# Kernel optimization log

Hardware: AMD Instinct MI355X
Metric: run time of the kernel (lower is better)

Reference implementation:

```python
import jax, jax.numpy as jnp
import numpy as np

V = [8192, 2048, 512, 128, 32]   # vertex counts per mesh level
S = 9                            # spiral length
T = 64                           # number of audio frames
OC = [32, 64, 64, 128]           # out_channels
LAT = 64                         # latent_channels


def _spiral_conv(x, idx, w, b):
    # x: [B, Vi, C], idx: [Vi, S] -> gather spiral neighborhoods, flatten, linear
    B = x.shape[0]
    n, s = idx.shape
    g = x[:, idx.reshape(-1), :].reshape(B, n, -1)  # [B, Vi, S*C]
    return g @ w + b


def _pool(x, row, col, val, out_size):
    # sparse COO matmul along vertex dim: out[b, r, :] += val * x[b, c, :]
    g = x[:, col, :] * val[None, :, None]
    return jnp.zeros((x.shape[0], out_size, x.shape[2]), x.dtype).at[:, row, :].add(g)


def setup_inputs():
    key = jax.random.key(0)
    keys = iter(jax.random.split(key, 80))
    def nrm(shape, scale=0.05):
        return jax.random.normal(next(keys), shape, jnp.float32) * scale
    inp = {}
    inp["hidden_states"] = jax.random.normal(next(keys), (1, T, 768), jnp.float32)
    inp["actor"] = jax.random.normal(next(keys), (1, V[0], 3), jnp.float32)
    inp["audio_w"] = nrm((768, LAT)); inp["audio_b"] = jnp.zeros((LAT,), jnp.float32)
    enc_dims = [(3 * S, OC[0]), (OC[0] * S, OC[1]), (OC[1] * S, OC[2]), (OC[2] * S, OC[3])]
    for i, (a, b) in enumerate(enc_dims):
        inp[f"enc{i}_w"] = nrm((a, b)); inp[f"enc{i}_b"] = jnp.zeros((b,), jnp.float32)
    inp["enc_lat_w"] = nrm((V[4] * OC[3], LAT)); inp["enc_lat_b"] = jnp.zeros((LAT,), jnp.float32)
    inp["dec_lin_w"] = nrm((2 * LAT, V[4] * OC[3])); inp["dec_lin_b"] = jnp.zeros((V[4] * OC[3],), jnp.float32)
    dec_dims = [(OC[3] * S, OC[3]), (OC[3] * S, OC[2]), (OC[2] * S, OC[1]), (OC[1] * S, OC[0])]
    for i, (a, b) in enumerate(dec_dims):
        inp[f"dec{i}_w"] = nrm((a, b)); inp[f"dec{i}_b"] = jnp.zeros((b,), jnp.float32)
    inp["dec_out_w"] = nrm((OC[0] * S, 3)); inp["dec_out_b"] = jnp.zeros((3,), jnp.float32)
    for i in range(4):
        inp[f"spiral{i}"] = jax.random.randint(next(keys), (V[i], S), 0, V[i])
    for i in range(4):
        vin, vout = V[i], V[i + 1]
        inp[f"down{i}_row"] = jnp.repeat(jnp.arange(vout), 3)
        inp[f"down{i}_col"] = jax.random.randint(next(keys), (3 * vout,), 0, vin)
        inp[f"down{i}_val"] = jax.random.uniform(next(keys), (3 * vout,), jnp.float32) / 3.0
        inp[f"up{i}_row"] = jnp.repeat(jnp.arange(vin), 3)
        inp[f"up{i}_col"] = jax.random.randint(next(keys), (3 * vin,), 0, vout)
        inp[f"up{i}_val"] = jax.random.uniform(next(keys), (3 * vin,), jnp.float32) / 3.0
    return inp


def reference(hidden_states, actor, audio_w, audio_b,
              enc0_w, enc0_b, enc1_w, enc1_b, enc2_w, enc2_b, enc3_w, enc3_b,
              enc_lat_w, enc_lat_b,
              dec_lin_w, dec_lin_b, dec0_w, dec0_b, dec1_w, dec1_b,
              dec2_w, dec2_b, dec3_w, dec3_b, dec_out_w, dec_out_b,
              spiral0, spiral1, spiral2, spiral3,
              down0_row, down0_col, down0_val, down1_row, down1_col, down1_val,
              down2_row, down2_col, down2_val, down3_row, down3_col, down3_val,
              up0_row, up0_col, up0_val, up1_row, up1_col, up1_val,
              up2_row, up2_col, up2_val, up3_row, up3_col, up3_val):
    spirals = [spiral0, spiral1, spiral2, spiral3]
    enc_p = [(enc0_w, enc0_b), (enc1_w, enc1_b), (enc2_w, enc2_b), (enc3_w, enc3_b)]
    dec_p = [(dec0_w, dec0_b), (dec1_w, dec1_b), (dec2_w, dec2_b), (dec3_w, dec3_b)]
    down = [(down0_row, down0_col, down0_val), (down1_row, down1_col, down1_val),
            (down2_row, down2_col, down2_val), (down3_row, down3_col, down3_val)]
    up = [(up0_row, up0_col, up0_val), (up1_row, up1_col, up1_val),
          (up2_row, up2_col, up2_val), (up3_row, up3_col, up3_val)]

    # ---- encode(actor): conv -> elu -> pool per level, then flatten linear ----
    x = actor  # [1, V0, 3]
    for i in range(4):
        w, b = enc_p[i]
        x = jax.nn.elu(_spiral_conv(x, spirals[i], w, b))
        r, c, v = down[i]
        x = _pool(x, r, c, v, V[i + 1])
    actor_emb = x.reshape(1, -1) @ enc_lat_w + enc_lat_b  # [1, LAT]

    # ---- audio embedding and latent concat ----
    audio_emb = hidden_states[0] @ audio_w + audio_b       # [T, LAT]
    latent = jnp.concatenate(
        [audio_emb, jnp.broadcast_to(actor_emb, audio_emb.shape)], axis=-1)  # [T, 2*LAT]

    # ---- decode all frames at once (original loops per frame; batched over T) ----
    x = (latent @ dec_lin_w + dec_lin_b).reshape(-1, V[4], OC[3])  # [T, V4, OC3]
    for i in range(4):
        lvl = 3 - i
        r, c, v = up[lvl]
        x = _pool(x, r, c, v, V[lvl])
        w, b = dec_p[i]
        x = jax.nn.elu(_spiral_conv(x, spirals[lvl], w, b))
    x = _spiral_conv(x, spirals[0], dec_out_w, dec_out_b)  # [T, V0, 3]
    return x + actor  # broadcast actor (displacement prediction), pred_sequence[1:]
```

## Files before the change

### kernel.cpp

```cpp
#include <hip/hip_runtime.h>
#include <hip/hip_bf16.h>

typedef __hip_bfloat16 bf16;
typedef __attribute__((ext_vector_type(8))) short short8v;
typedef __attribute__((ext_vector_type(16))) float f32x16;

__device__ __forceinline__ float tof(float v){ return v; }
__device__ __forceinline__ float tof(bf16 v){ return __bfloat162float(v); }
__device__ __forceinline__ void sto(float* p, float v){ *p = v; }
__device__ __forceinline__ void sto(bf16* p, float v){ *p = __float2bfloat16(v); }
__device__ __forceinline__ short f2bs(float f){ bf16 h = __float2bfloat16(f); return *(short*)&h; }
__device__ __forceinline__ float bsu2f(short s){
    return __uint_as_float(((unsigned)(unsigned short)s) << 16);
}

__device__ __forceinline__ void sto4(float* p, float4 v){ *(float4*)p = v; }
__device__ __forceinline__ void sto4(bf16* p, float4 v){
    short4 s; s.x=f2bs(v.x); s.y=f2bs(v.y); s.z=f2bs(v.z); s.w=f2bs(v.w);
    *(short4*)p = s;
}

__device__ __forceinline__ void swz_t(int b, int bs, int& t, int& rem){
    int x = b & 7, k = b >> 3;
    t = x*8 + (k >> bs);
    rem = k & ((1 << bs) - 1);
}

__global__ __launch_bounds__(256) void k_prep(
    const float* __restrict__ w0, const float* __restrict__ w1,
    const float* __restrict__ w2, const float* __restrict__ w3,
    const float* __restrict__ w4,
    short* __restrict__ wt0, short* __restrict__ wt1,
    short* __restrict__ wt2, short* __restrict__ wt3,
    short* __restrict__ wt4,
    const float* __restrict__ hs, const float* __restrict__ aw,
    const float* __restrict__ ab, float* __restrict__ aemb)
{
    __shared__ float red[4][64];
    int b = blockIdx.x, tid = threadIdx.x;
    if (b < 1080){
        const float* w; short* wt; int K, nsh, i;
        if      (b < 576) { w = w0; wt = wt0; K = 1152; nsh = 7; i = b*256 + tid; }
        else if (b < 864) { w = w1; wt = wt1; K = 1152; nsh = 6; i = (b-576)*256 + tid; }
        else if (b < 1008){ w = w2; wt = wt2; K = 576;  nsh = 6; i = (b-864)*256 + tid; }
        else              { w = w3; wt = wt3; K = 576;  nsh = 5; i = (b-1008)*256 + tid; }
        int k = i >> nsh, n = i & ((1 << nsh) - 1);
        wt[n*K + k] = f2bs(w[i]);
    } else if (b < 1116){
        int i = (b - 1080)*256 + tid;
        int k = i >> 5, n = i & 31;
        wt4[n*288 + k] = (n < 3) ? f2bs(w4[k*3 + n]) : (short)0;
    } else {
        int t = b - 1116;
        int kg = tid >> 6, l = tid & 63;
        const float* h = hs + t*768;
        float acc = 0.f;
        int k0 = kg*192;
        #pragma unroll 8
        for (int k = k0; k < k0 + 192; k++) acc += h[k] * aw[k*64 + l];
        red[kg][l] = acc;
        __syncthreads();
        if (kg == 0)
            aemb[t*64 + l] = red[0][l] + red[1][l] + red[2][l] + red[3][l] + ab[l];
    }
}

__global__ __launch_bounds__(256) void k_enclat(const float* __restrict__ flat,
    const float* __restrict__ w, const float* __restrict__ b, float* __restrict__ out)
{
    __shared__ float red[256];
    int l = blockIdx.x, tid = threadIdx.x;
    float acc = 0.f;
    for (int k = tid; k < 4096; k += 256) acc += flat[k] * w[k*64 + l];
    red[tid] = acc; __syncthreads();
    for (int s = 128; s > 0; s >>= 1){ if (tid < s) red[tid] += red[tid+s]; __syncthreads(); }
    if (tid == 0) out[l] = red[0] + b[l];
}

__global__ __launch_bounds__(256) void k_declin4(const float* __restrict__ ae,
    const float* __restrict__ pe, const float* __restrict__ w, const float* __restrict__ b,
    bf16* __restrict__ out)
{
    int n4 = blockIdx.x*256 + threadIdx.x;
    int t = blockIdx.y;
    float4 acc = *(const float4*)&b[n4*4];
    const float* a = ae + t*64;
    #pragma unroll 4
    for (int k = 0; k < 64; k++){
        float av = a[k];
        float4 wv = *(const float4*)&w[(size_t)k*4096 + n4*4];
        acc.x += av*wv.x; acc.y += av*wv.y; acc.z += av*wv.z; acc.w += av*wv.w;
    }
    #pragma unroll 4
    for (int k = 0; k < 64; k++){
        float pv = pe[k];
        float4 wv = *(const float4*)&w[(size_t)(64+k)*4096 + n4*4];
        acc.x += pv*wv.x; acc.y += pv*wv.y; acc.z += pv*wv.z; acc.w += pv*wv.w;
    }
    sto4(&out[(size_t)t*4096 + n4*4], acc);
}

__global__ __launch_bounds__(256) void k_pool4(const float* __restrict__ xin,
    const int* __restrict__ col, const float* __restrict__ val, float* __restrict__ out,
    int total4, int c4mask, int cs, int vomask, int vos, int Vi)
{
    int i = blockIdx.x*256 + threadIdx.x;
    if (i >= total4) return;
    int c4 = i & c4mask;
    int rv = i >> cs;
    int r  = rv & vomask;
    int t  = rv >> vos;
    int C  = (c4mask + 1) << 2;
    const float* xt = xin + (size_t)t * Vi * C;
    int r3 = 3*r;
    int j0 = col[r3], j1 = col[r3+1], j2 = col[r3+2];
    float v0 = val[r3], v1 = val[r3+1], v2 = val[r3+2];
    int c = c4 << 2;
    float4 a = *(const float4*)&xt[(size_t)j0*C + c];
    float4 b = *(const float4*)&xt[(size_t)j1*C + c];
    float4 d = *(const float4*)&xt[(size_t)j2*C + c];
    float4 o;
    o.x = v0*a.x + v1*b.x + v2*d.x;
    o.y = v0*a.y + v1*b.y + v2*d.y;
    o.z = v0*a.z + v1*b.z + v2*d.z;
    o.w = v0*a.w + v1*b.w + v2*d.w;
    sto4(&out[(size_t)i << 2], o);
}

__global__ __launch_bounds__(256) void k_poolb(const bf16* __restrict__ xin,
    const int* __restrict__ col, const float* __restrict__ val, bf16* __restrict__ out,
    int c8mask, int cs, int vom, int vshin, int cshift, int bs, int ept8)
{
    int t, rem; swz_t(blockIdx.x, bs, t, rem);
    int il = rem*256 + threadIdx.x;
    int c8 = il & c8mask;
    int r  = (il >> cs) & vom;
    size_t i = (size_t)t * ept8 + il;
    const bf16* xt = xin + ((size_t)t << (vshin + cshift));
    int r3 = 3*r;
    int j0 = col[r3], j1 = col[r3+1], j2 = col[r3+2];
    float v0 = val[r3], v1 = val[r3+1], v2 = val[r3+2];
    int c = c8 << 3;
    short8v a = *(const short8v*)&xt[((size_t)j0 << cshift) + c];
    short8v b = *(const short8v*)&xt[((size_t)j1 << cshift) + c];
    short8v d = *(const short8v*)&xt[((size_t)j2 << cshift) + c];
    short8v o;
    #pragma unroll
    for (int q = 0; q < 8; q++)
        o[q] = f2bs(v0*bsu2f(a[q]) + v1*bsu2f(b[q]) + v2*bsu2f(d[q]));
    *(short8v*)&out[i << 3] = o;
}

template<int KTOT, int CSHIFT, int NTOT, int MTILES, typename TOUT>
__global__ __launch_bounds__(256) void k_conv_p(
    const bf16* __restrict__ xin, const int* __restrict__ spiral,
    const short* __restrict__ wt, const float* __restrict__ bias, TOUT* __restrict__ out,
    int vshift, int bs, int nbshift)
{
    constexpr int MT   = 128*MTILES;
    constexpr int NCH  = KTOT >> 6;
    constexpr int CSUB = CSHIFT - 6;
    constexpr int AU   = MT*8/256;
    __shared__ short lds_a[MT*72];
    __shared__ short lds_b[32*72];
    const int tid = threadIdx.x;
    const int lane = tid & 63;
    const int wv = tid >> 6;
    const int col = lane & 31;
    const int half = lane >> 5;

    int t, rem; swz_t(blockIdx.x, bs, t, rem);
    const int nb = rem & ((1 << nbshift) - 1);
    const int vt = rem >> nbshift;
    const int mbase = vt*MT;
    const size_t xslab = (size_t)t << (vshift + CSHIFT);

    short8v pa[AU];
    short8v pb;
    const int am = tid >> 3;
    const int ak = (tid & 7) << 3;
    const int bn = tid >> 3;
    const int bk = (tid & 7) << 3;

    auto issue = [&](int ch){
        int s = ch >> CSUB;
        int coff = ((ch & ((1 << CSUB) - 1)) << 6) + ak;
        #pragma unroll
        for (int u = 0; u < AU; u++){
            int j = spiral[(mbase + am + u*32)*9 + s];
            pa[u] = *(const short8v*)&xin[xslab + ((size_t)j << CSHIFT) + coff];
        }
        pb = *(const short8v*)&wt[(size_t)(nb*32 + bn)*KTOT + (ch << 6) + bk];
    };
    auto commit = [&](){
        #pragma unroll
        for (int u = 0; u < AU; u++)
            *(short8v*)&lds_a[(am + u*32)*72 + ak] = pa[u];
        *(short8v*)&lds_b[bn*72 + bk] = pb;
    };

    f32x16 acc[MTILES];
    {
        float bv = bias[nb*32 + col];
        #pragma unroll
        for (int h = 0; h < MTILES; h++)
            #pragma unroll
            for (int r = 0; r < 16; r++) acc[h][r] = bv;
    }

    issue(0);
    commit();
    __syncthreads();
    for (int ch = 0; ch < NCH; ch++){
        if (ch + 1 < NCH) issue(ch + 1);
        #pragma unroll
        for (int ks = 0; ks < 4; ks++){
            short8v b = *(short8v*)&lds_b[col*72 + ks*16 + half*8];
            #pragma unroll
            for (int h = 0; h < MTILES; h++){
                short8v a = *(short8v*)&lds_a[(h*128 + wv*32 + col)*72 + ks*16 + half*8];
                acc[h] = __builtin_amdgcn_mfma_f32_32x32x16_bf16(a, b, acc[h], 0, 0, 0);
            }
        }
        __syncthreads();
        if (ch + 1 < NCH){
            commit();
            __syncthreads();
        }
    }
    #pragma unroll
    for (int h = 0; h < MTILES; h++){
        size_t mb = ((size_t)t << vshift) + mbase + h*128 + wv*32;
        #pragma unroll
        for (int r = 0; r < 16; r++){
            int row = (r & 3) + 8*(r >> 2) + 4*half;
            float vv = acc[h][r];
            vv = vv > 0.f ? vv : __expf(vv) - 1.f;
            sto(&out[(mb + row)*NTOT + nb*32 + col], vv);
        }
    }
}

__global__ __launch_bounds__(256) void k_outmfma(
    const bf16* __restrict__ xin, const int* __restrict__ spiral,
    const short* __restrict__ wt, const float* __restrict__ bias,
    const float* __restrict__ actor, float* __restrict__ out)
{
    __shared__ short lds_a[256*36];
    __shared__ short lds_b[32*36];
    const int tid = threadIdx.x;
    const int lane = tid & 63;
    const int wv = tid >> 6;
    const int col = lane & 31;
    const int half = lane >> 5;

    int t, rem; swz_t(blockIdx.x, 5, t, rem);
    const int mbase = rem*256;
    const size_t xslab = (size_t)t << 18;

    short8v pa[4];
    short8v pb;
    const int am = tid >> 2;
    const int ak = (tid & 3) << 3;

    auto issue = [&](int s){
        #pragma unroll
        for (int u = 0; u < 4; u++){
            int j = spiral[(mbase + am + u*64)*9 + s];
            pa[u] = *(const short8v*)&xin[xslab + ((size_t)j << 5) + ak];
        }
        if (tid < 128)
            pb = *(const short8v*)&wt[am*288 + s*32 + ak];
    };
    auto commit = [&](){
        #pragma unroll
        for (int u = 0; u < 4; u++)
            *(short8v*)&lds_a[(am + u*64)*36 + ak] = pa[u];
        if (tid < 128)
            *(short8v*)&lds_b[am*36 + ak] = pb;
    };

    f32x16 acc[2];
    {
        float bv = (col < 3) ? bias[col] : 0.f;
        #pragma unroll
        for (int h = 0; h < 2; h++)
            #pragma unroll
            for (int r = 0; r < 16; r++) acc[h][r] = bv;
    }

    issue(0); commit(); __syncthreads();
    for (int s = 0; s < 9; s++){
        if (s + 1 < 9) issue(s + 1);
        #pragma unroll
        for (int ks = 0; ks < 2; ks++){
            short8v b = *(short8v*)&lds_b[col*36 + ks*16 + half*8];
            #pragma unroll
            for (int h = 0; h < 2; h++){
                short8v a = *(short8v*)&lds_a[(h*128 + wv*32 + col)*36 + ks*16 + half*8];
                acc[h] = __builtin_amdgcn_mfma_f32_32x32x16_bf16(a, b, acc[h], 0, 0, 0);
            }
        }
        __syncthreads();
        if (s + 1 < 9){ commit(); __syncthreads(); }
    }
    if (col < 3){
        #pragma unroll
        for (int h = 0; h < 2; h++){
            int rowb = mbase + h*128 + wv*32;
            #pragma unroll
            for (int r = 0; r < 16; r++){
                int row = rowb + (r & 3) + 8*(r >> 2) + 4*half;
                out[(((size_t)t << 13) + row)*3 + col] = acc[h][r] + actor[row*3 + col];
            }
        }
    }
}

template<typename TIN>
__global__ __launch_bounds__(256) void k_conv(const TIN* __restrict__ xin,
    const int* __restrict__ spiral, const float* __restrict__ w, const float* __restrict__ bias,
    float* __restrict__ out, int TV, int V, int vshift, int C, int O2, int o2shift,
    int K, int KP, int MT)
{
    extern __shared__ float lds[];
    const int S = 9;
    int tid = threadIdx.x;
    int O = O2 << 1;
    int gmbase = blockIdx.x * MT;

    int total = MT * K;
    for (int e = tid; e < total; e += 256){
        int m = e / K, k = e - m*K;
        int gm = gmbase + m;
        if (gm < TV){
            int t = gm >> vshift, v = gm & (V-1);
            int s = k / C, c = k - s*C;
            int jj = spiral[v*S + s];
            lds[m*KP + k] = tof(xin[((size_t)t*V + jj)*C + c]);
        }
    }
    __syncthreads();

    int m = tid >> o2shift;
    int o = tid & (O2 - 1);
    int gm = gmbase + m;
    if (gm >= TV) return;
    const float* g  = lds + m*KP;
    const float* wp = w + 2*o;
    float acc0 = bias[2*o];
    float acc1 = bias[2*o+1];
    int K4 = K & ~3;
    for (int k = 0; k < K4; k += 4){
        float4 g4 = *(const float4*)(g + k);
        float2 w0 = *(const float2*)(wp + (size_t)k    *O);
        float2 w1 = *(const float2*)(wp + (size_t)(k+1)*O);
        float2 w2 = *(const float2*)(wp + (size_t)(k+2)*O);
        float2 w3 = *(const float2*)(wp + (size_t)(k+3)*O);
        acc0 += g4.x*w0.x + g4.y*w1.x + g4.z*w2.x + g4.w*w3.x;
        acc1 += g4.x*w0.y + g4.y*w1.y + g4.z*w2.y + g4.w*w3.y;
    }
    for (int k = K4; k < K; k++){
        float gv = g[k];
        acc0 += gv * wp[(size_t)k*O];
        acc1 += gv * wp[(size_t)k*O + 1];
    }
    acc0 = acc0 > 0.f ? acc0 : __expf(acc0) - 1.f;
    acc1 = acc1 > 0.f ? acc1 : __expf(acc1) - 1.f;
    float2 r; r.x = acc0; r.y = acc1;
    *(float2*)(out + (size_t)gm*O + 2*o) = r;
}

extern "C" void kernel_launch(void* const* d_in, const int* in_sizes, int n_in,
                              void* d_out, int out_size, void* d_ws, size_t ws_size,
                              hipStream_t stream)
{
    (void)n_in; (void)out_size; (void)ws_size;
    const float* hs        = (const float*)d_in[0];
    const float* actor     = (const float*)d_in[1];
    const float* audio_w   = (const float*)d_in[2];
    const float* audio_b   = (const float*)d_in[3];
    const float* enc_w[4]  = {(const float*)d_in[4],(const float*)d_in[6],(const float*)d_in[8],(const float*)d_in[10]};
    const float* enc_b[4]  = {(const float*)d_in[5],(const float*)d_in[7],(const float*)d_in[9],(const float*)d_in[11]};
    const float* enc_lat_w = (const float*)d_in[12];
    const float* enc_lat_b = (const float*)d_in[13];
    const float* dec_lin_w = (const float*)d_in[14];
    const float* dec_lin_b = (const float*)d_in[15];
    const float* dec_w[4]  = {(const float*)d_in[16],(const float*)d_in[18],(const float*)d_in[20],(const float*)d_in[22]};
    const float* dec_b[4]  = {(const float*)d_in[17],(const float*)d_in[19],(const float*)d_in[21],(const float*)d_in[23]};
    const float* dec_out_w = (const float*)d_in[24];
    const float* dec_out_b = (const float*)d_in[25];
    const int*   spiral[4] = {(const int*)d_in[26],(const int*)d_in[27],(const int*)d_in[28],(const int*)d_in[29]};

    const int* dcol[4]; const float* dval[4]; const int* ucol[4]; const float* uval[4];
    bool interleaved = (in_sizes[33] == 3*8192);
    for (int i = 0; i < 4; i++){
        if (interleaved){
            int b = 30 + 6*i;
            dcol[i] = (const int*)d_in[b+1]; dval[i] = (const float*)d_in[b+2];
            ucol[i] = (const int*)d_in[b+4]; uval[i] = (const float*)d_in[b+5];
        } else {
            dcol[i] = (const int*)d_in[31+3*i]; dval[i] = (const float*)d_in[32+3*i];
            ucol[i] = (const int*)d_in[43+3*i]; uval[i] = (const float*)d_in[44+3*i];
        }
    }

    char* ws = (char*)d_ws;
    size_t off = 0;
    auto alloc = [&](size_t bytes)->char* {
        char* p = ws + off; off += (bytes + 255) & ~(size_t)255; return p;
    };
    float* encX0 = (float*)alloc((size_t)262144*4);
    float* encP0 = (float*)alloc((size_t)65536*4);
    float* encX1 = (float*)alloc((size_t)131072*4);
    float* encP1 = (float*)alloc((size_t)32768*4);
    float* encX2 = (float*)alloc((size_t)32768*4);
    float* encP2 = (float*)alloc((size_t)8192*4);
    float* encX3 = (float*)alloc((size_t)16384*4);
    float* encP3 = (float*)alloc((size_t)4096*4);
    float* aemb  = (float*)alloc((size_t)4096*4);
    float* pemb  = (float*)alloc((size_t)64*4);
    short* wt0   = (short*)alloc((size_t)147456*2);
    short* wt1   = (short*)alloc((size_t)73728*2);
    short* wt2   = (short*)alloc((size_t)36864*2);
    short* wt3   = (short*)alloc((size_t)18432*2);
    short* wt4   = (short*)alloc((size_t)9216*2);
    bf16*  Pb    = (bf16*)alloc((size_t)36*1048576);
    bf16*  Qb    = (bf16*)alloc((size_t)68*1048576);

    k_prep<<<1180,256,0,stream>>>(dec_w[0], dec_w[1], dec_w[2], dec_w[3], dec_out_w,
                                  wt0, wt1, wt2, wt3, wt4, hs, audio_w, audio_b, aemb);

    k_conv<float><<<512,256, 16*28*4, stream>>>(actor, spiral[0], enc_w[0], enc_b[0], encX0, 8192, 8192,13,   3,16,4,  27,  28,16);
    k_pool4<<<64,256,0,stream>>>(encX0, dcol[0], dval[0], encP0, 16384, 7,3, 2047,11, 8192);
    k_conv<float><<<256,256, 8*292*4, stream>>>(encP0, spiral[1], enc_w[1], enc_b[1], encX1, 2048, 2048,11,  32,32,5, 288, 292, 8);
    k_pool4<<<32,256,0,stream>>>(encX1, dcol[1], dval[1], encP1, 8192, 15,4, 511,9, 2048);
    k_conv<float><<<64,256, 8*580*4, stream>>>(encP1, spiral[2], enc_w[2], enc_b[2], encX2, 512, 512,9,  64,32,5, 576, 580, 8);
    k_pool4<<<8,256,0,stream>>>(encX2, dcol[2], dval[2], encP2, 2048, 15,4, 127,7, 512);
    k_conv<float><<<32,256, 4*580*4, stream>>>(encP2, spiral[3], enc_w[3], enc_b[3], encX3, 128, 128,7,  64,64,6, 576, 580, 4);
    k_pool4<<<4,256,0,stream>>>(encX3, dcol[3], dval[3], encP3, 1024, 31,5, 31,5, 128);
    k_enclat<<<64,256,0,stream>>>(encP3, enc_lat_w, enc_lat_b, pemb);

    k_declin4<<<dim3(4,64),256,0,stream>>>(aemb, pemb, dec_lin_w, dec_lin_b, Pb);

    k_poolb<<<512,256,0,stream>>>(Pb, ucol[3], uval[3], Qb, 15,4, 127, 5,7, 3, 2048);
    k_conv_p<1152,7,128,1,bf16><<<256,256,0,stream>>>(Qb, spiral[3], wt0, dec_b[0], Pb, 7, 2, 2);

    k_poolb<<<2048,256,0,stream>>>(Pb, ucol[2], uval[2], Qb, 15,4, 511, 7,7, 5, 8192);
    k_conv_p<1152,7,64,2,bf16><<<256,256,0,stream>>>(Qb, spiral[2], wt1, dec_b[1], Pb, 9, 2, 1);

    k_poolb<<<4096,256,0,stream>>>(Pb, ucol[1], uval[1], Qb, 7,3, 2047, 9,6, 6, 16384);
    k_conv_p<576,6,64,2,bf16><<<1024,256,0,stream>>>(Qb, spiral[1], wt2, dec_b[2], Pb, 11, 4, 1);

    k_poolb<<<16384,256,0,stream>>>(Pb, ucol[0], uval[0], Qb, 7,3, 8191, 11,6, 8, 65536);
    k_conv_p<576,6,32,2,bf16><<<2048,256,0,stream>>>(Qb, spiral[0], wt3, dec_b[3], Pb, 13, 5, 0);

    k_outmfma<<<2048,256,0,stream>>>(Pb, spiral[0], wt4, dec_out_b, actor, (float*)d_out);
}
```

Measured before the change: 462.6 us.

## Double-buffer LDS in decoder spiral conv and shrink M tile to 128

Replaces the decoder spiral-conv GEMM kernel with a version that keeps two LDS stages and two register prefetch stages, so global gathers for chunk ch+2 are in flight while chunk ch is multiplied. This removes one of the two barriers per K chunk. The M tile is fixed at 128 rows (one MFMA tile per wave), which doubles the grid for the larger levels to raise parallelism, at the cost of fetching each weight tile twice as often and using more registers and LDS per block.

```diff
diff --git a/kernel.cpp b/kernel.cpp
--- a/kernel.cpp
+++ b/kernel.cpp
@@ -151,18 +151,16 @@
     *(short8v*)&out[i << 3] = o;
 }
 
-template<int KTOT, int CSHIFT, int NTOT, int MTILES, typename TOUT>
-__global__ __launch_bounds__(256) void k_conv_p(
+template<int KTOT, int CSHIFT, int NTOT, typename TOUT>
+__global__ __launch_bounds__(256) void k_conv_p2(
     const bf16* __restrict__ xin, const int* __restrict__ spiral,
     const short* __restrict__ wt, const float* __restrict__ bias, TOUT* __restrict__ out,
     int vshift, int bs, int nbshift)
 {
-    constexpr int MT   = 128*MTILES;
     constexpr int NCH  = KTOT >> 6;
     constexpr int CSUB = CSHIFT - 6;
-    constexpr int AU   = MT*8/256;
-    __shared__ short lds_a[MT*72];
-    __shared__ short lds_b[32*72];
+    __shared__ short lds_a[2*128*72];
+    __shared__ short lds_b[2*32*72];
     const int tid = threadIdx.x;
     const int lane = tid & 63;
     const int wv = tid >> 6;
@@ -172,72 +170,67 @@
     int t, rem; swz_t(blockIdx.x, bs, t, rem);
     const int nb = rem & ((1 << nbshift) - 1);
     const int vt = rem >> nbshift;
-    const int mbase = vt*MT;
+    const int mbase = vt*128;
     const size_t xslab = (size_t)t << (vshift + CSHIFT);
 
-    short8v pa[AU];
-    short8v pb;
     const int am = tid >> 3;
     const int ak = (tid & 7) << 3;
     const int bn = tid >> 3;
     const int bk = (tid & 7) << 3;
 
-    auto issue = [&](int ch){
+    short8v pa[2][4];
+    short8v pb[2];
+
+    auto issue = [&](int ch, int st){
         int s = ch >> CSUB;
         int coff = ((ch & ((1 << CSUB) - 1)) << 6) + ak;
         #pragma unroll
-        for (int u = 0; u < AU; u++){
+        for (int u = 0; u < 4; u++){
             int j = spiral[(mbase + am + u*32)*9 + s];
-            pa[u] = *(const short8v*)&xin[xslab + ((size_t)j << CSHIFT) + coff];
-        }
-        pb = *(const short8v*)&wt[(size_t)(nb*32 + bn)*KTOT + (ch << 6) + bk];
+            pa[st][u] = *(const short8v*)&xin[xslab + ((size_t)j << CSHIFT) + coff];
+        }
+        pb[st] = *(const short8v*)&wt[(size_t)(nb*32 + bn)*KTOT + (ch << 6) + bk];
     };
-    auto commit = [&](){
-        #pragma unroll
-        for (int u = 0; u < AU; u++)
-            *(short8v*)&lds_a[(am + u*32)*72 + ak] = pa[u];
-        *(short8v*)&lds_b[bn*72 + bk] = pb;
+    auto commit = [&](int ch, int st){
+        short* la = lds_a + (ch & 1)*(128*72);
+        short* lb = lds_b + (ch & 1)*(32*72);
+        #pragma unroll
+        for (int u = 0; u < 4; u++)
+            *(short8v*)&la[(am + u*32)*72 + ak] = pa[st][u];
+        *(short8v*)&lb[bn*72 + bk] = pb[st];
     };
 
-    f32x16 acc[MTILES];
+    f32x16 acc;
     {
         float bv = bias[nb*32 + col];
         #pragma unroll
-        for (int h = 0; h < MTILES; h++)
-            #pragma unroll
-            for (int r = 0; r < 16; r++) acc[h][r] = bv;
-    }
-
-    issue(0);
-    commit();
+        for (int r = 0; r < 16; r++) acc[r] = bv;
+    }
+
+    issue(0, 0);
+    if (NCH > 1) issue(1, 1);
+    commit(0, 0);
     __syncthreads();
     for (int ch = 0; ch < NCH; ch++){
-        if (ch + 1 < NCH) issue(ch + 1);
+        if (ch + 2 < NCH) issue(ch + 2, ch & 1);
+        const short* la = lds_a + (ch & 1)*(128*72);
+        const short* lb = lds_b + (ch & 1)*(32*72);
         #pragma unroll
         for (int ks = 0; ks < 4; ks++){
-            short8v b = *(short8v*)&lds_b[col*72 + ks*16 + half*8];
-            #pragma unroll
-            for (int h = 0; h < MTILES; h++){
-                short8v a = *(short8v*)&lds_a[(h*128 + wv*32 + col)*72 + ks*16 + half*8];
-                acc[h] = __builtin_amdgcn_mfma_f32_32x32x16_bf16(a, b, acc[h], 0, 0, 0);
-            }
-        }
+            short8v b = *(const short8v*)&lb[col*72 + ks*16 + half*8];
+            short8v a = *(const short8v*)&la[(wv*32 + col)*72 + ks*16 + half*8];
+            acc = __builtin_amdgcn_mfma_f32_32x32x16_bf16(a, b, acc, 0, 0, 0);
+        }
+        if (ch + 1 < NCH) commit(ch + 1, (ch + 1) & 1);
         __syncthreads();
-        if (ch + 1 < NCH){
-            commit();
-            __syncthreads();
-        }
-    }
+    }
+    size_t mb = ((size_t)t << vshift) + mbase + wv*32;
     #pragma unroll
-    for (int h = 0; h < MTILES; h++){
-        size_t mb = ((size_t)t << vshift) + mbase + h*128 + wv*32;
-        #pragma unroll
-        for (int r = 0; r < 16; r++){
-            int row = (r & 3) + 8*(r >> 2) + 4*half;
-            float vv = acc[h][r];
-            vv = vv > 0.f ? vv : __expf(vv) - 1.f;
-            sto(&out[(mb + row)*NTOT + nb*32 + col], vv);
-        }
+    for (int r = 0; r < 16; r++){
+        int row = (r & 3) + 8*(r >> 2) + 4*half;
+        float vv = acc[r];
+        vv = vv > 0.f ? vv : __expf(vv) - 1.f;
+        sto(&out[(mb + row)*NTOT + nb*32 + col], vv);
     }
 }
 
@@ -444,16 +437,16 @@
     k_declin4<<<dim3(4,64),256,0,stream>>>(aemb, pemb, dec_lin_w, dec_lin_b, Pb);
 
     k_poolb<<<512,256,0,stream>>>(Pb, ucol[3], uval[3], Qb, 15,4, 127, 5,7, 3, 2048);
-    k_conv_p<1152,7,128,1,bf16><<<256,256,0,stream>>>(Qb, spiral[3], wt0, dec_b[0], Pb, 7, 2, 2);
+    k_conv_p2<1152,7,128,bf16><<<256,256,0,stream>>>(Qb, spiral[3], wt0, dec_b[0], Pb, 7, 2, 2);
 
     k_poolb<<<2048,256,0,stream>>>(Pb, ucol[2], uval[2], Qb, 15,4, 511, 7,7, 5, 8192);
-    k_conv_p<1152,7,64,2,bf16><<<256,256,0,stream>>>(Qb, spiral[2], wt1, dec_b[1], Pb, 9, 2, 1);
+    k_conv_p2<1152,7,64,bf16><<<512,256,0,stream>>>(Qb, spiral[2], wt1, dec_b[1], Pb, 9, 3, 1);
 
     k_poolb<<<4096,256,0,stream>>>(Pb, ucol[1], uval[1], Qb, 7,3, 2047, 9,6, 6, 16384);
-    k_conv_p<576,6,64,2,bf16><<<1024,256,0,stream>>>(Qb, spiral[1], wt2, dec_b[2], Pb, 11, 4, 1);
+    k_conv_p2<576,6,64,bf16><<<2048,256,0,stream>>>(Qb, spiral[1], wt2, dec_b[2], Pb, 11, 5, 1);
 
     k_poolb<<<16384,256,0,stream>>>(Pb, ucol[0], uval[0], Qb, 7,3, 8191, 11,6, 8, 65536);
-    k_conv_p<576,6,32,2,bf16><<<2048,256,0,stream>>>(Qb, spiral[0], wt3, dec_b[3], Pb, 13, 5, 0);
+    k_conv_p2<576,6,32,bf16><<<4096,256,0,stream>>>(Qb, spiral[0], wt3, dec_b[3], Pb, 13, 6, 0);
 
     k_outmfma<<<2048,256,0,stream>>>(Pb, spiral[0], wt4, dec_out_b, actor, (float*)d_out);
 }
```

After: 435.5 us. 5.9% less time.
